# Optimization experiments

Measured on AMD Instinct MI355X. Metric: run time of the kernel, lower is better.

The kernel has to match this reference:

```python
import jax, jax.numpy as jnp
import numpy as np

WS = 7          # window_size[0]
UP = 2          # hardcoded upscale
WS2 = WS * UP   # 14
NUM_HEADS = 6
DIM = 192
HEAD_DIM = DIM // NUM_HEADS
SCALE = HEAD_DIM ** -0.5
TABLE_SIZE = (WS + WS2 - 1) ** 2  # 400


def _relative_position_index():
    # Mirrors the torch __init__ index construction (meshgrid 'ij').
    ch = np.arange(WS)
    cw = np.arange(WS2)
    r1, c1 = np.meshgrid(ch, ch, indexing='ij')   # (7,7)
    r2, c2 = np.meshgrid(cw, cw, indexing='ij')   # (14,14)
    r1, c1 = r1.reshape(-1), c1.reshape(-1)       # (49,)
    r2, c2 = r2.reshape(-1), c2.reshape(-1)       # (196,)
    rel_row = r1[:, None] - r2[None, :] + (WS2 - 1)          # (49,196) in [0,19]
    rel_col = c1[:, None] - c2[None, :] + (WS2 - 1)
    idx = rel_row * (WS + WS2 - 1) + rel_col                 # (49,196) in [0,399]
    return jnp.asarray(idx, dtype=jnp.int32)

REL_INDEX = _relative_position_index()


def setup_inputs() -> dict:
    key = jax.random.key(0)
    ks = jax.random.split(key, 9)
    B, N, N2, C = 1024, WS * WS, WS2 * WS2, DIM
    std = 0.02
    return {
        'x1': jax.random.normal(ks[0], (B, N, C), jnp.float32),
        'x2': jax.random.normal(ks[1], (B, N2, C), jnp.float32),
        # Linear weights stored as (in, out) so y = x @ W + b
        'qkv_w': jax.random.normal(ks[2], (C, C), jnp.float32) * std,
        'qkv_b': jnp.zeros((C,), jnp.float32),
        'qkv2_w': jax.random.normal(ks[3], (C, 2 * C), jnp.float32) * std,
        'qkv2_b': jnp.zeros((2 * C,), jnp.float32),
        'proj_w': jax.random.normal(ks[4], (C, C), jnp.float32) * std,
        'proj_b': jnp.zeros((C,), jnp.float32),
        'bias_table': jax.random.normal(ks[5], (TABLE_SIZE, NUM_HEADS), jnp.float32) * std,
    }


def reference(x1, x2, qkv_w, qkv_b, qkv2_w, qkv2_b, proj_w, proj_b, bias_table):
    B, N, C = x1.shape
    _, N2, _ = x2.shape
    H, D = NUM_HEADS, HEAD_DIM

    q = (x1 @ qkv_w + qkv_b).reshape(B, N, H, D).transpose(0, 2, 1, 3)        # [B,H,N,D]
    kv = (x2 @ qkv2_w + qkv2_b).reshape(B, N2, 2, H, D).transpose(2, 0, 3, 1, 4)
    k, v = kv[0], kv[1]                                                        # [B,H,N2,D]

    attn = jnp.einsum('bhnd,bhmd->bhnm', q * SCALE, k)                         # [B,H,N,N2]
    bias = bias_table[REL_INDEX].transpose(2, 0, 1)                            # [H,N,N2]
    attn = jax.nn.softmax(attn + bias[None], axis=-1)

    out = jnp.einsum('bhnm,bhmd->bhnd', attn, v).transpose(0, 2, 1, 3).reshape(B, N, C)
    return out @ proj_w + proj_b
```

## Files before the change

kernel.cpp:

```cpp
#include <hip/hip_runtime.h>


typedef __attribute__((ext_vector_type(8))) short bf16x8;
typedef __attribute__((ext_vector_type(4))) float f32x4;

#define MFMA16(a, b, c) __builtin_amdgcn_mfma_f32_16x16x32_bf16((a), (b), (c), 0, 0, 0)

#define WS_QKVT  0
#define WS_QKV2T 36864
#define WS_PROJH 110592
#define WS_PROJL 147456
#define BIAS_F32 92160

#define SCALE_Q 0.17677669529663687f

__device__ __forceinline__ unsigned short f2bf(float f) {
  unsigned int u = __float_as_uint(f);
  u += 0x7fffu + ((u >> 16) & 1u);
  return (unsigned short)(u >> 16);
}
__device__ __forceinline__ float bf2f(unsigned short s) {
  return __uint_as_float(((unsigned int)s) << 16);
}
__device__ __forceinline__ bf16x8 cvt8(const float* __restrict__ p) {
  union { bf16x8 v; unsigned short s[8]; } U;
  float4 v0 = *(const float4*)p;
  float4 v1 = *(const float4*)(p + 4);
  U.s[0] = f2bf(v0.x); U.s[1] = f2bf(v0.y); U.s[2] = f2bf(v0.z); U.s[3] = f2bf(v0.w);
  U.s[4] = f2bf(v1.x); U.s[5] = f2bf(v1.y); U.s[6] = f2bf(v1.z); U.s[7] = f2bf(v1.w);
  return U.v;
}

__global__ void prep_kernel(const float* __restrict__ qkv_w,
                            const float* __restrict__ qkv2_w,
                            const float* __restrict__ proj_w,
                            const float* __restrict__ btab,
                            unsigned short* __restrict__ ws) {
  int t = blockIdx.x * 256 + threadIdx.x;
  if (t < 36864) {
    int k = t / 192, n = t % 192;
    ws[WS_QKVT + n * 192 + k] = f2bf(qkv_w[t]);
  } else if (t < 110592) {
    int u = t - 36864;
    int k = u / 384, n = u % 384;
    ws[WS_QKV2T + n * 192 + k] = f2bf(qkv2_w[u]);
  } else if (t < 147456) {
    int u = t - 110592;
    int k = u / 192, n = u % 192;
    float p = proj_w[u];
    unsigned short hi = f2bf(p);
    ws[WS_PROJH + n * 192 + k] = hi;
    ws[WS_PROJL + n * 192 + k] = f2bf(p - bf2f(hi));
  } else if (t < 233472) {
    int u = t - 147456;
    int h = u / 14336;
    int r2 = u - h * 14336;
    int key = r2 >> 6, qrow = r2 & 63;
    float v;
    if (key >= 196)      v = -1e30f;
    else if (qrow >= 49) v = 0.f;
    else {
      int jh = key / 14, jw = key - 14 * jh;
      int ih = qrow / 7, iw = qrow - 7 * ih;
      v = btab[((ih - jh + 13) * 20 + (iw - jw + 13)) * 6 + h];
    }
    ((float*)ws)[BIAS_F32 + u] = v;
  }
}

__launch_bounds__(256, 4)
__global__ void fused_attn_kernel(const float* __restrict__ x1,
                                  const float* __restrict__ x2,
                                  const float* __restrict__ qkv_b,
                                  const float* __restrict__ qkv2_b,
                                  const unsigned short* __restrict__ ws,
                                  float* __restrict__ out) {
  __shared__ __align__(16) char smem[36608];
  unsigned short* ksm = (unsigned short*)(smem);
  unsigned short* qhm = (unsigned short*)(smem + 16640);
  unsigned short* vtm = (unsigned short*)(smem + 21760);

  const int tid  = threadIdx.x;
  const int wave = tid >> 6;
  const int lane = tid & 63;
  const int l16  = lane & 15;
  const int quad = lane >> 4;

  const int logical = (blockIdx.x & 7) * 768 + (blockIdx.x >> 3);
  const int win  = logical / 6;
  const int h    = logical - win * 6;

  const float* x1b = x1 + (size_t)win * (49 * 192);
  const float* x2b = x2 + (size_t)win * (196 * 192);
  const float* bbt = (const float*)ws + BIAS_F32 + h * 14336;

  {
    int d = tid >> 3, c = tid & 7;
    *(unsigned int*)(vtm + d * 232 + 208 + c * 2) = 0u;
  }

  {
    f32x4 qa0{0.f, 0.f, 0.f, 0.f}, qa1{0.f, 0.f, 0.f, 0.f};
    const int mq = wave * 16 + l16;
    const bool mv = (mq < 49);
#pragma unroll
    for (int kk = 0; kk < 6; ++kk) {
      bf16x8 a = mv ? cvt8(x1b + mq * 192 + kk * 32 + quad * 8)
                    : bf16x8{0, 0, 0, 0, 0, 0, 0, 0};
      const unsigned short* wq = ws + WS_QKVT + (h * 32 + l16) * 192 + kk * 32 + quad * 8;
      qa0 = MFMA16(a, *(const bf16x8*)(wq), qa0);
      qa1 = MFMA16(a, *(const bf16x8*)(wq + 16 * 192), qa1);
    }
    const float b0 = qkv_b[h * 32 + l16];
    const float b1 = qkv_b[h * 32 + 16 + l16];
#pragma unroll
    for (int r = 0; r < 4; ++r) {
      const int row = wave * 16 + quad * 4 + r;
      qhm[row * 40 + l16]      = f2bf((qa0[r] + b0) * SCALE_Q);
      qhm[row * 40 + 16 + l16] = f2bf((qa1[r] + b1) * SCALE_Q);
    }
  }
  const float bk0 = qkv2_b[h * 32 + l16];
  const float bk1 = qkv2_b[h * 32 + 16 + l16];
  const float bv0 = qkv2_b[192 + h * 32 + l16];
  const float bv1 = qkv2_b[192 + h * 32 + 16 + l16];
  {
    f32x4 ka0[3], ka1[3], va0[3], va1[3];
#pragma unroll
    for (int ti = 0; ti < 3; ++ti) {
      ka0[ti] = f32x4{0.f, 0.f, 0.f, 0.f}; ka1[ti] = f32x4{0.f, 0.f, 0.f, 0.f};
      va0[ti] = f32x4{0.f, 0.f, 0.f, 0.f}; va1[ti] = f32x4{0.f, 0.f, 0.f, 0.f};
    }
#pragma unroll 2
    for (int kk = 0; kk < 6; ++kk) {
      const unsigned short* wk = ws + WS_QKV2T + (h * 32 + l16) * 192 + kk * 32 + quad * 8;
      bf16x8 w0 = *(const bf16x8*)(wk);
      bf16x8 w1 = *(const bf16x8*)(wk + 16 * 192);
      bf16x8 w2 = *(const bf16x8*)(wk + 192 * 192);
      bf16x8 w3 = *(const bf16x8*)(wk + 208 * 192);
#pragma unroll
      for (int ti = 0; ti < 3; ++ti) {
        bf16x8 a = cvt8(x2b + ((ti * 4 + wave) * 16 + l16) * 192 + kk * 32 + quad * 8);
        ka0[ti] = MFMA16(a, w0, ka0[ti]);
        ka1[ti] = MFMA16(a, w1, ka1[ti]);
        va0[ti] = MFMA16(a, w2, va0[ti]);
        va1[ti] = MFMA16(a, w3, va1[ti]);
      }
    }
#pragma unroll
    for (int ti = 0; ti < 3; ++ti) {
#pragma unroll
      for (int r = 0; r < 4; ++r) {
        const int row = (ti * 4 + wave) * 16 + quad * 4 + r;
        ksm[row * 40 + l16]        = f2bf(ka0[ti][r] + bk0);
        ksm[row * 40 + 16 + l16]   = f2bf(ka1[ti][r] + bk1);
        vtm[l16 * 232 + row]        = f2bf(va0[ti][r] + bv0);
        vtm[(16 + l16) * 232 + row] = f2bf(va1[ti][r] + bv1);
      }
    }
  }
  if (wave == 0) {
    f32x4 a0{0.f, 0.f, 0.f, 0.f}, a1{0.f, 0.f, 0.f, 0.f};
    f32x4 a2{0.f, 0.f, 0.f, 0.f}, a3{0.f, 0.f, 0.f, 0.f};
    const int m = 192 + l16;
    const bool mv = (m < 196);
#pragma unroll 2
    for (int kk = 0; kk < 6; ++kk) {
      bf16x8 a = mv ? cvt8(x2b + m * 192 + kk * 32 + quad * 8)
                    : bf16x8{0, 0, 0, 0, 0, 0, 0, 0};
      const unsigned short* wk = ws + WS_QKV2T + (h * 32 + l16) * 192 + kk * 32 + quad * 8;
      a0 = MFMA16(a, *(const bf16x8*)(wk), a0);
      a1 = MFMA16(a, *(const bf16x8*)(wk + 16 * 192), a1);
      a2 = MFMA16(a, *(const bf16x8*)(wk + 192 * 192), a2);
      a3 = MFMA16(a, *(const bf16x8*)(wk + 208 * 192), a3);
    }
#pragma unroll
    for (int r = 0; r < 4; ++r) {
      const int row = 192 + quad * 4 + r;
      const bool rv = (row < 196);
      ksm[row * 40 + l16]        = rv ? f2bf(a0[r] + bk0) : (unsigned short)0;
      ksm[row * 40 + 16 + l16]   = rv ? f2bf(a1[r] + bk1) : (unsigned short)0;
      vtm[l16 * 232 + row]        = rv ? f2bf(a2[r] + bv0) : (unsigned short)0;
      vtm[(16 + l16) * 232 + row] = rv ? f2bf(a3[r] + bv1) : (unsigned short)0;
    }
  }
  __syncthreads();

  f32x4 lg[13];
  {
    bf16x8 aq = *(const bf16x8*)(qhm + (wave * 16 + l16) * 40 + quad * 8);
#pragma unroll
    for (int nt = 0; nt < 13; ++nt)
      lg[nt] = *(const f32x4*)(bbt + (nt * 16 + l16) * 64 + wave * 16 + quad * 4);
#pragma unroll
    for (int nt = 0; nt < 13; ++nt)
      lg[nt] = MFMA16(aq, *(const bf16x8*)(ksm + (nt * 16 + l16) * 40 + quad * 8), lg[nt]);
#pragma unroll
    for (int r = 0; r < 4; ++r) {
      float mx = lg[0][r];
#pragma unroll
      for (int nt = 1; nt < 13; ++nt) mx = fmaxf(mx, lg[nt][r]);
      mx = fmaxf(mx, __shfl_xor(mx, 1));
      mx = fmaxf(mx, __shfl_xor(mx, 2));
      mx = fmaxf(mx, __shfl_xor(mx, 4));
      mx = fmaxf(mx, __shfl_xor(mx, 8));
      float s = 0.f;
#pragma unroll
      for (int nt = 0; nt < 13; ++nt) {
        float p = __expf(lg[nt][r] - mx);
        lg[nt][r] = p;
        s += p;
      }
      s += __shfl_xor(s, 1);
      s += __shfl_xor(s, 2);
      s += __shfl_xor(s, 4);
      s += __shfl_xor(s, 8);
      const float inv = 1.f / s;
#pragma unroll
      for (int nt = 0; nt < 13; ++nt) lg[nt][r] *= inv;
    }
  }
  __syncthreads();

  unsigned short* ps = (unsigned short*)(smem + wave * 4352);
  f32x4 o0{0.f, 0.f, 0.f, 0.f}, o1{0.f, 0.f, 0.f, 0.f};
#pragma unroll
  for (int r = 0; r < 4; ++r) {
    const int row = quad * 4 + r;
#pragma unroll
    for (int nt = 0; nt < 8; ++nt)
      ps[row * 136 + nt * 16 + l16] = f2bf(lg[nt][r]);
  }
#pragma unroll
  for (int kk = 0; kk < 4; ++kk) {
    bf16x8 a  = *(const bf16x8*)(ps + l16 * 136 + kk * 32 + quad * 8);
    bf16x8 b0 = *(const bf16x8*)(vtm + l16 * 232 + kk * 32 + quad * 8);
    bf16x8 b1 = *(const bf16x8*)(vtm + (16 + l16) * 232 + kk * 32 + quad * 8);
    o0 = MFMA16(a, b0, o0);
    o1 = MFMA16(a, b1, o1);
  }
#pragma unroll
  for (int r = 0; r < 4; ++r) {
    const int row = quad * 4 + r;
#pragma unroll
    for (int nt = 8; nt < 13; ++nt)
      ps[row * 104 + (nt - 8) * 16 + l16] = f2bf(lg[nt][r]);
    ps[row * 104 + 80 + l16] = 0;
  }
#pragma unroll
  for (int kk = 0; kk < 3; ++kk) {
    bf16x8 a  = *(const bf16x8*)(ps + l16 * 104 + kk * 32 + quad * 8);
    bf16x8 b0 = *(const bf16x8*)(vtm + l16 * 232 + (4 + kk) * 32 + quad * 8);
    bf16x8 b1 = *(const bf16x8*)(vtm + (16 + l16) * 232 + (4 + kk) * 32 + quad * 8);
    o0 = MFMA16(a, b0, o0);
    o1 = MFMA16(a, b1, o1);
  }
  {
    float* ob = out + (size_t)win * 9408 + h * 32;
#pragma unroll
    for (int r = 0; r < 4; ++r) {
      const int row = wave * 16 + quad * 4 + r;
      if (row < 49) {
        float* op = ob + row * 192;
        op[l16]      = o0[r];
        op[16 + l16] = o1[r];
      }
    }
  }
}

__launch_bounds__(256, 4)
__global__ void proj_kernel(const float* __restrict__ proj_b,
                            const unsigned short* __restrict__ ws,
                            float* __restrict__ out) {
  const int tid  = threadIdx.x;
  const int wave = tid >> 6;
  const int lane = tid & 63;
  const int l16  = lane & 15;
  const int quad = lane >> 4;
  const int rowg = (wave & 1) * 16;
  const int nth  = (wave >> 1) * 6;
  const size_t base = (size_t)blockIdx.x * 32 * 192;

  f32x4 pacc[6];
#pragma unroll
  for (int nt = 0; nt < 6; ++nt) pacc[nt] = f32x4{0.f, 0.f, 0.f, 0.f};

  const float* ap0 = out + base + (rowg + l16) * 192;
#pragma unroll 2
  for (int kk = 0; kk < 6; ++kk) {
    const int k0 = kk * 32 + quad * 8;
    float4 v0 = *(const float4*)(ap0 + k0);
    float4 v1 = *(const float4*)(ap0 + k0 + 4);
    float f[8] = {v0.x, v0.y, v0.z, v0.w, v1.x, v1.y, v1.z, v1.w};
    union { bf16x8 v; unsigned short s[8]; } H, L;
#pragma unroll
    for (int j = 0; j < 8; ++j) {
      H.s[j] = f2bf(f[j]);
      L.s[j] = f2bf(f[j] - bf2f(H.s[j]));
    }
#pragma unroll
    for (int nt = 0; nt < 6; ++nt) {
      bf16x8 bh = *(const bf16x8*)(ws + WS_PROJH + ((nth + nt) * 16 + l16) * 192 + k0);
      bf16x8 bl = *(const bf16x8*)(ws + WS_PROJL + ((nth + nt) * 16 + l16) * 192 + k0);
      pacc[nt] = MFMA16(H.v, bh, pacc[nt]);
      pacc[nt] = MFMA16(H.v, bl, pacc[nt]);
      pacc[nt] = MFMA16(L.v, bh, pacc[nt]);
    }
  }
  __syncthreads();
#pragma unroll
  for (int nt = 0; nt < 6; ++nt) {
    const float pb = proj_b[(nth + nt) * 16 + l16];
#pragma unroll
    for (int r = 0; r < 4; ++r) {
      const int row = rowg + quad * 4 + r;
      out[base + row * 192 + (nth + nt) * 16 + l16] = pacc[nt][r] + pb;
    }
  }
}

extern "C" void kernel_launch(void* const* d_in, const int* in_sizes, int n_in,
                              void* d_out, int out_size, void* d_ws, size_t ws_size,
                              hipStream_t stream) {
  const float* x1     = (const float*)d_in[0];
  const float* x2     = (const float*)d_in[1];
  const float* qkv_w  = (const float*)d_in[2];
  const float* qkv_b  = (const float*)d_in[3];
  const float* qkv2_w = (const float*)d_in[4];
  const float* qkv2_b = (const float*)d_in[5];
  const float* proj_w = (const float*)d_in[6];
  const float* proj_b = (const float*)d_in[7];
  const float* btab   = (const float*)d_in[8];
  unsigned short* ws  = (unsigned short*)d_ws;
  float* out          = (float*)d_out;
  (void)in_sizes; (void)n_in; (void)out_size; (void)ws_size;

  prep_kernel<<<dim3(912), dim3(256), 0, stream>>>(qkv_w, qkv2_w, proj_w, btab, ws);
  fused_attn_kernel<<<dim3(6144), dim3(256), 0, stream>>>(x1, x2, qkv_b, qkv2_b,
                                                          ws, out);
  proj_kernel<<<dim3(1568), dim3(256), 0, stream>>>(proj_b, ws, out);
}
```

Before: 574.7 us.

## Pre-cast inputs to bf16 in workspace and store attention output as bf16 hi/lo

Adds a cast kernel that converts x1 and x2 to bf16 once into the workspace, so each per-head attention block reads half-size bf16 activations instead of reloading and converting fp32 six times. The attention output is written as a bf16 hi/lo split pair, which the projection kernel consumes directly. The path is gated on workspace size, falling back to the original fp32 kernels otherwise. It adds a separate pass over the inputs and a large workspace footprint.

```diff
diff --git a/kernel.cpp b/kernel.cpp
--- a/kernel.cpp
+++ b/kernel.cpp
@@ -11,6 +11,11 @@
 #define WS_PROJH 110592
 #define WS_PROJL 147456
 #define BIAS_F32 92160
+#define X1C_U16  524288
+#define X2C_U16  10158080
+#define OH_U16   48693248
+#define OL_U16   58327040
+#define WS_NEEDED 135921664ull
 
 #define SCALE_Q 0.17677669529663687f
 
@@ -68,13 +73,25 @@
   }
 }
 
+__launch_bounds__(256, 8)
+__global__ void cast_kernel(const float* __restrict__ x1,
+                            const float* __restrict__ x2,
+                            unsigned short* __restrict__ ws) {
+  const int T = 6021120;
+  for (int i = blockIdx.x * 256 + threadIdx.x; i < T; i += gridDim.x * 256) {
+    if (i < 1204224) {
+      *(bf16x8*)(ws + X1C_U16 + (size_t)i * 8) = cvt8(x1 + (size_t)i * 8);
+    } else {
+      size_t j = (size_t)(i - 1204224);
+      *(bf16x8*)(ws + X2C_U16 + j * 8) = cvt8(x2 + j * 8);
+    }
+  }
+}
+
 __launch_bounds__(256, 4)
-__global__ void fused_attn_kernel(const float* __restrict__ x1,
-                                  const float* __restrict__ x2,
-                                  const float* __restrict__ qkv_b,
+__global__ void fused_attn_kernel(const float* __restrict__ qkv_b,
                                   const float* __restrict__ qkv2_b,
-                                  const unsigned short* __restrict__ ws,
-                                  float* __restrict__ out) {
+                                  unsigned short* __restrict__ ws) {
   __shared__ __align__(16) char smem[36608];
   unsigned short* ksm = (unsigned short*)(smem);
   unsigned short* qhm = (unsigned short*)(smem + 16640);
@@ -90,6 +107,256 @@
   const int win  = logical / 6;
   const int h    = logical - win * 6;
 
+  const unsigned short* x1c = ws + X1C_U16 + (size_t)win * (49 * 192);
+  const unsigned short* x2c = ws + X2C_U16 + (size_t)win * (196 * 192);
+  const float* bbt = (const float*)ws + BIAS_F32 + h * 14336;
+
+  {
+    int d = tid >> 3, c = tid & 7;
+    *(unsigned int*)(vtm + d * 232 + 208 + c * 2) = 0u;
+  }
+
+  {
+    f32x4 qa0{0.f, 0.f, 0.f, 0.f}, qa1{0.f, 0.f, 0.f, 0.f};
+    const int mq = wave * 16 + l16;
+    const bool mv = (mq < 49);
+#pragma unroll
+    for (int kk = 0; kk < 6; ++kk) {
+      bf16x8 a = mv ? *(const bf16x8*)(x1c + mq * 192 + kk * 32 + quad * 8)
+                    : bf16x8{0, 0, 0, 0, 0, 0, 0, 0};
+      const unsigned short* wq = ws + WS_QKVT + (h * 32 + l16) * 192 + kk * 32 + quad * 8;
+      qa0 = MFMA16(a, *(const bf16x8*)(wq), qa0);
+      qa1 = MFMA16(a, *(const bf16x8*)(wq + 16 * 192), qa1);
+    }
+    const float b0 = qkv_b[h * 32 + l16];
+    const float b1 = qkv_b[h * 32 + 16 + l16];
+#pragma unroll
+    for (int r = 0; r < 4; ++r) {
+      const int row = wave * 16 + quad * 4 + r;
+      qhm[row * 40 + l16]      = f2bf((qa0[r] + b0) * SCALE_Q);
+      qhm[row * 40 + 16 + l16] = f2bf((qa1[r] + b1) * SCALE_Q);
+    }
+  }
+  const float bk0 = qkv2_b[h * 32 + l16];
+  const float bk1 = qkv2_b[h * 32 + 16 + l16];
+  const float bv0 = qkv2_b[192 + h * 32 + l16];
+  const float bv1 = qkv2_b[192 + h * 32 + 16 + l16];
+  {
+    f32x4 ka0[3], ka1[3], va0[3], va1[3];
+#pragma unroll
+    for (int ti = 0; ti < 3; ++ti) {
+      ka0[ti] = f32x4{0.f, 0.f, 0.f, 0.f}; ka1[ti] = f32x4{0.f, 0.f, 0.f, 0.f};
+      va0[ti] = f32x4{0.f, 0.f, 0.f, 0.f}; va1[ti] = f32x4{0.f, 0.f, 0.f, 0.f};
+    }
+#pragma unroll 2
+    for (int kk = 0; kk < 6; ++kk) {
+      const unsigned short* wk = ws + WS_QKV2T + (h * 32 + l16) * 192 + kk * 32 + quad * 8;
+      bf16x8 w0 = *(const bf16x8*)(wk);
+      bf16x8 w1 = *(const bf16x8*)(wk + 16 * 192);
+      bf16x8 w2 = *(const bf16x8*)(wk + 192 * 192);
+      bf16x8 w3 = *(const bf16x8*)(wk + 208 * 192);
+#pragma unroll
+      for (int ti = 0; ti < 3; ++ti) {
+        bf16x8 a = *(const bf16x8*)(x2c + ((ti * 4 + wave) * 16 + l16) * 192 + kk * 32 + quad * 8);
+        ka0[ti] = MFMA16(a, w0, ka0[ti]);
+        ka1[ti] = MFMA16(a, w1, ka1[ti]);
+        va0[ti] = MFMA16(a, w2, va0[ti]);
+        va1[ti] = MFMA16(a, w3, va1[ti]);
+      }
+    }
+#pragma unroll
+    for (int ti = 0; ti < 3; ++ti) {
+#pragma unroll
+      for (int r = 0; r < 4; ++r) {
+        const int row = (ti * 4 + wave) * 16 + quad * 4 + r;
+        ksm[row * 40 + l16]        = f2bf(ka0[ti][r] + bk0);
+        ksm[row * 40 + 16 + l16]   = f2bf(ka1[ti][r] + bk1);
+        vtm[l16 * 232 + row]        = f2bf(va0[ti][r] + bv0);
+        vtm[(16 + l16) * 232 + row] = f2bf(va1[ti][r] + bv1);
+      }
+    }
+  }
+  if (wave == 0) {
+    f32x4 a0{0.f, 0.f, 0.f, 0.f}, a1{0.f, 0.f, 0.f, 0.f};
+    f32x4 a2{0.f, 0.f, 0.f, 0.f}, a3{0.f, 0.f, 0.f, 0.f};
+    const int m = 192 + l16;
+    const bool mv = (m < 196);
+#pragma unroll 2
+    for (int kk = 0; kk < 6; ++kk) {
+      bf16x8 a = mv ? *(const bf16x8*)(x2c + m * 192 + kk * 32 + quad * 8)
+                    : bf16x8{0, 0, 0, 0, 0, 0, 0, 0};
+      const unsigned short* wk = ws + WS_QKV2T + (h * 32 + l16) * 192 + kk * 32 + quad * 8;
+      a0 = MFMA16(a, *(const bf16x8*)(wk), a0);
+      a1 = MFMA16(a, *(const bf16x8*)(wk + 16 * 192), a1);
+      a2 = MFMA16(a, *(const bf16x8*)(wk + 192 * 192), a2);
+      a3 = MFMA16(a, *(const bf16x8*)(wk + 208 * 192), a3);
+    }
+#pragma unroll
+    for (int r = 0; r < 4; ++r) {
+      const int row = 192 + quad * 4 + r;
+      const bool rv = (row < 196);
+      ksm[row * 40 + l16]        = rv ? f2bf(a0[r] + bk0) : (unsigned short)0;
+      ksm[row * 40 + 16 + l16]   = rv ? f2bf(a1[r] + bk1) : (unsigned short)0;
+      vtm[l16 * 232 + row]        = rv ? f2bf(a2[r] + bv0) : (unsigned short)0;
+      vtm[(16 + l16) * 232 + row] = rv ? f2bf(a3[r] + bv1) : (unsigned short)0;
+    }
+  }
+  __syncthreads();
+
+  f32x4 lg[13];
+  {
+    bf16x8 aq = *(const bf16x8*)(qhm + (wave * 16 + l16) * 40 + quad * 8);
+#pragma unroll
+    for (int nt = 0; nt < 13; ++nt)
+      lg[nt] = *(const f32x4*)(bbt + (nt * 16 + l16) * 64 + wave * 16 + quad * 4);
+#pragma unroll
+    for (int nt = 0; nt < 13; ++nt)
+      lg[nt] = MFMA16(aq, *(const bf16x8*)(ksm + (nt * 16 + l16) * 40 + quad * 8), lg[nt]);
+#pragma unroll
+    for (int r = 0; r < 4; ++r) {
+      float mx = lg[0][r];
+#pragma unroll
+      for (int nt = 1; nt < 13; ++nt) mx = fmaxf(mx, lg[nt][r]);
+      mx = fmaxf(mx, __shfl_xor(mx, 1));
+      mx = fmaxf(mx, __shfl_xor(mx, 2));
+      mx = fmaxf(mx, __shfl_xor(mx, 4));
+      mx = fmaxf(mx, __shfl_xor(mx, 8));
+      float s = 0.f;
+#pragma unroll
+      for (int nt = 0; nt < 13; ++nt) {
+        float p = __expf(lg[nt][r] - mx);
+        lg[nt][r] = p;
+        s += p;
+      }
+      s += __shfl_xor(s, 1);
+      s += __shfl_xor(s, 2);
+      s += __shfl_xor(s, 4);
+      s += __shfl_xor(s, 8);
+      const float inv = 1.f / s;
+#pragma unroll
+      for (int nt = 0; nt < 13; ++nt) lg[nt][r] *= inv;
+    }
+  }
+  __syncthreads();
+
+  unsigned short* ps = (unsigned short*)(smem + wave * 4352);
+  f32x4 o0{0.f, 0.f, 0.f, 0.f}, o1{0.f, 0.f, 0.f, 0.f};
+#pragma unroll
+  for (int r = 0; r < 4; ++r) {
+    const int row = quad * 4 + r;
+#pragma unroll
+    for (int nt = 0; nt < 8; ++nt)
+      ps[row * 136 + nt * 16 + l16] = f2bf(lg[nt][r]);
+  }
+#pragma unroll
+  for (int kk = 0; kk < 4; ++kk) {
+    bf16x8 a  = *(const bf16x8*)(ps + l16 * 136 + kk * 32 + quad * 8);
+    bf16x8 b0 = *(const bf16x8*)(vtm + l16 * 232 + kk * 32 + quad * 8);
+    bf16x8 b1 = *(const bf16x8*)(vtm + (16 + l16) * 232 + kk * 32 + quad * 8);
+    o0 = MFMA16(a, b0, o0);
+    o1 = MFMA16(a, b1, o1);
+  }
+#pragma unroll
+  for (int r = 0; r < 4; ++r) {
+    const int row = quad * 4 + r;
+#pragma unroll
+    for (int nt = 8; nt < 13; ++nt)
+      ps[row * 104 + (nt - 8) * 16 + l16] = f2bf(lg[nt][r]);
+    ps[row * 104 + 80 + l16] = 0;
+  }
+#pragma unroll
+  for (int kk = 0; kk < 3; ++kk) {
+    bf16x8 a  = *(const bf16x8*)(ps + l16 * 104 + kk * 32 + quad * 8);
+    bf16x8 b0 = *(const bf16x8*)(vtm + l16 * 232 + (4 + kk) * 32 + quad * 8);
+    bf16x8 b1 = *(const bf16x8*)(vtm + (16 + l16) * 232 + (4 + kk) * 32 + quad * 8);
+    o0 = MFMA16(a, b0, o0);
+    o1 = MFMA16(a, b1, o1);
+  }
+  {
+    unsigned short* oh = ws + OH_U16 + (size_t)win * 49 * 192 + h * 32;
+    unsigned short* ol = ws + OL_U16 + (size_t)win * 49 * 192 + h * 32;
+#pragma unroll
+    for (int r = 0; r < 4; ++r) {
+      const int row = wave * 16 + quad * 4 + r;
+      if (row < 49) {
+        float v0 = o0[r], v1 = o1[r];
+        unsigned short h0 = f2bf(v0), h1 = f2bf(v1);
+        oh[row * 192 + l16]      = h0;
+        ol[row * 192 + l16]      = f2bf(v0 - bf2f(h0));
+        oh[row * 192 + 16 + l16] = h1;
+        ol[row * 192 + 16 + l16] = f2bf(v1 - bf2f(h1));
+      }
+    }
+  }
+}
+
+__launch_bounds__(256, 4)
+__global__ void proj_kernel(const float* __restrict__ proj_b,
+                            const unsigned short* __restrict__ ws,
+                            float* __restrict__ out) {
+  const int tid  = threadIdx.x;
+  const int wave = tid >> 6;
+  const int lane = tid & 63;
+  const int l16  = lane & 15;
+  const int quad = lane >> 4;
+  const int rowg = (wave & 1) * 16;
+  const int nth  = (wave >> 1) * 6;
+  const size_t rbase = (size_t)blockIdx.x * 32;
+
+  const unsigned short* ah = ws + OH_U16 + (rbase + rowg + l16) * 192;
+  const unsigned short* al = ws + OL_U16 + (rbase + rowg + l16) * 192;
+
+  f32x4 pacc[6];
+#pragma unroll
+  for (int nt = 0; nt < 6; ++nt) pacc[nt] = f32x4{0.f, 0.f, 0.f, 0.f};
+
+#pragma unroll 2
+  for (int kk = 0; kk < 6; ++kk) {
+    const int k0 = kk * 32 + quad * 8;
+    bf16x8 AH = *(const bf16x8*)(ah + k0);
+    bf16x8 AL = *(const bf16x8*)(al + k0);
+#pragma unroll
+    for (int nt = 0; nt < 6; ++nt) {
+      bf16x8 bh = *(const bf16x8*)(ws + WS_PROJH + ((nth + nt) * 16 + l16) * 192 + k0);
+      bf16x8 bl = *(const bf16x8*)(ws + WS_PROJL + ((nth + nt) * 16 + l16) * 192 + k0);
+      pacc[nt] = MFMA16(AH, bh, pacc[nt]);
+      pacc[nt] = MFMA16(AH, bl, pacc[nt]);
+      pacc[nt] = MFMA16(AL, bh, pacc[nt]);
+    }
+  }
+#pragma unroll
+  for (int nt = 0; nt < 6; ++nt) {
+    const float pb = proj_b[(nth + nt) * 16 + l16];
+#pragma unroll
+    for (int r = 0; r < 4; ++r) {
+      const int row = rowg + quad * 4 + r;
+      out[(rbase + row) * 192 + (nth + nt) * 16 + l16] = pacc[nt][r] + pb;
+    }
+  }
+}
+
+__launch_bounds__(256, 4)
+__global__ void fused_attn_f32_kernel(const float* __restrict__ x1,
+                                      const float* __restrict__ x2,
+                                      const float* __restrict__ qkv_b,
+                                      const float* __restrict__ qkv2_b,
+                                      const unsigned short* __restrict__ ws,
+                                      float* __restrict__ out) {
+  __shared__ __align__(16) char smem[36608];
+  unsigned short* ksm = (unsigned short*)(smem);
+  unsigned short* qhm = (unsigned short*)(smem + 16640);
+  unsigned short* vtm = (unsigned short*)(smem + 21760);
+
+  const int tid  = threadIdx.x;
+  const int wave = tid >> 6;
+  const int lane = tid & 63;
+  const int l16  = lane & 15;
+  const int quad = lane >> 4;
+
+  const int logical = (blockIdx.x & 7) * 768 + (blockIdx.x >> 3);
+  const int win  = logical / 6;
+  const int h    = logical - win * 6;
+
   const float* x1b = x1 + (size_t)win * (49 * 192);
   const float* x2b = x2 + (size_t)win * (196 * 192);
   const float* bbt = (const float*)ws + BIAS_F32 + h * 14336;
@@ -98,7 +365,6 @@
     int d = tid >> 3, c = tid & 7;
     *(unsigned int*)(vtm + d * 232 + 208 + c * 2) = 0u;
   }
-
   {
     f32x4 qa0{0.f, 0.f, 0.f, 0.f}, qa1{0.f, 0.f, 0.f, 0.f};
     const int mq = wave * 16 + l16;
@@ -270,9 +536,9 @@
 }
 
 __launch_bounds__(256, 4)
-__global__ void proj_kernel(const float* __restrict__ proj_b,
-                            const unsigned short* __restrict__ ws,
-                            float* __restrict__ out) {
+__global__ void proj_inplace_kernel(const float* __restrict__ proj_b,
+                                    const unsigned short* __restrict__ ws,
+                                    float* __restrict__ out) {
   const int tid  = threadIdx.x;
   const int wave = tid >> 6;
   const int lane = tid & 63;
@@ -334,10 +600,16 @@
   const float* btab   = (const float*)d_in[8];
   unsigned short* ws  = (unsigned short*)d_ws;
   float* out          = (float*)d_out;
-  (void)in_sizes; (void)n_in; (void)out_size; (void)ws_size;
+  (void)in_sizes; (void)n_in; (void)out_size;
 
   prep_kernel<<<dim3(912), dim3(256), 0, stream>>>(qkv_w, qkv2_w, proj_w, btab, ws);
-  fused_attn_kernel<<<dim3(6144), dim3(256), 0, stream>>>(x1, x2, qkv_b, qkv2_b,
-                                                          ws, out);
-  proj_kernel<<<dim3(1568), dim3(256), 0, stream>>>(proj_b, ws, out);
-}
+  if (ws_size >= WS_NEEDED) {
+    cast_kernel<<<dim3(2048), dim3(256), 0, stream>>>(x1, x2, ws);
+    fused_attn_kernel<<<dim3(6144), dim3(256), 0, stream>>>(qkv_b, qkv2_b, ws);
+    proj_kernel<<<dim3(1568), dim3(256), 0, stream>>>(proj_b, ws, out);
+  } else {
+    fused_attn_f32_kernel<<<dim3(6144), dim3(256), 0, stream>>>(x1, x2, qkv_b,
+                                                                qkv2_b, ws, out);
+    proj_inplace_kernel<<<dim3(1568), dim3(256), 0, stream>>>(proj_b, ws, out);
+  }
+}
```

Result: no change. 567.0 us (-1.3%).
